# Optimization experiments

Hardware: AMD Instinct MI355X
Metric: run time of the kernel (lower is better)

The kernel has to match this reference:

```python
import jax, jax.numpy as jnp
import numpy as np

E = 1024
H = 16
D = E // H  # head_dim = 64
FF = 4 * E
EPS = 1e-5


def layernorm(x, g, b):
    mu = jnp.mean(x, axis=-1, keepdims=True)
    var = jnp.var(x, axis=-1, keepdims=True)
    return (x - mu) * jax.lax.rsqrt(var + EPS) * g + b


def setup_inputs() -> dict:
    key = jax.random.key(0)
    ks = jax.random.split(key, 12)
    s = 1.0 / np.sqrt(E)
    sf = 1.0 / np.sqrt(FF)
    return {
        "x": jax.random.normal(ks[0], (2, 2048, E), dtype=jnp.float32),
        "wq": jax.random.uniform(ks[1], (E, E), jnp.float32, -s, s),
        "wk": jax.random.uniform(ks[2], (E, E), jnp.float32, -s, s),
        "wv": jax.random.uniform(ks[3], (E, E), jnp.float32, -s, s),
        "wo": jax.random.uniform(ks[4], (E, E), jnp.float32, -s, s),
        "bo": jax.random.uniform(ks[5], (E,), jnp.float32, -s, s),
        "g1": jnp.ones((E,), jnp.float32),
        "b1": jnp.zeros((E,), jnp.float32),
        "w1": jax.random.uniform(ks[6], (FF, E), jnp.float32, -s, s),
        "bf1": jax.random.uniform(ks[7], (FF,), jnp.float32, -s, s),
        "w2": jax.random.uniform(ks[8], (E, FF), jnp.float32, -sf, sf),
        "bf2": jax.random.uniform(ks[9], (E,), jnp.float32, -sf, sf),
        "g2": jnp.ones((E,), jnp.float32),
        "b2": jnp.zeros((E,), jnp.float32),
    }


def reference(x, wq, wk, wv, wo, bo, g1, b1, w1, bf1, w2, bf2, g2, b2):
    B, L, _ = x.shape
    # projections (torch Linear: x @ W.T)
    q = (x @ wq.T).reshape(B, L, H, D).transpose(0, 2, 1, 3)  # (B,H,L,D)
    k = (x @ wk.T).reshape(B, L, H, D).transpose(0, 2, 1, 3)
    v = (x @ wv.T).reshape(B, L, H, D).transpose(0, 2, 1, 3)
    scores = jnp.einsum('bhqd,bhkd->bhqk', q, k) / np.sqrt(D)
    attn = jax.nn.softmax(scores, axis=-1)
    ctx = jnp.einsum('bhqk,bhkd->bhqd', attn, v)
    ctx = ctx.transpose(0, 2, 1, 3).reshape(B, L, E)
    attn_out = ctx @ wo.T + bo
    h = layernorm(x + attn_out, g1, b1)
    ff = jax.nn.gelu(h @ w1.T + bf1, approximate=False) @ w2.T + bf2
    return layernorm(h + ff, g2, b2)
```

## Files before the change

### kernel.cpp

```cpp
#include <hip/hip_runtime.h>
#include <hip/hip_bf16.h>
#include <stdint.h>

typedef __bf16 bf16x8 __attribute__((ext_vector_type(8)));
typedef float  f32x4  __attribute__((ext_vector_type(4)));
typedef unsigned short u16;
typedef u16 u16x8 __attribute__((ext_vector_type(8)));

__device__ __forceinline__ u16 f2b(float f) {
  uint32_t u = __builtin_bit_cast(uint32_t, f);
  u += 0x7fffu + ((u >> 16) & 1u);
  return (u16)(u >> 16);
}

__device__ __forceinline__ f32x4 mfma16(bf16x8 a, bf16x8 b, f32x4 c) {
  return __builtin_amdgcn_mfma_f32_16x16x32_bf16(a, b, c, 0, 0, 0);
}

__device__ __forceinline__ void gload_lds16(const void* g, void* l) {
  __builtin_amdgcn_global_load_lds(
      (const __attribute__((address_space(1))) void*)g,
      (__attribute__((address_space(3))) void*)l, 16, 0, 0);
}

__global__ void f2b_all(const float* __restrict__ x,  const float* __restrict__ wq,
                        const float* __restrict__ wk, const float* __restrict__ wv,
                        const float* __restrict__ wo, const float* __restrict__ w1,
                        const float* __restrict__ w2,
                        u16* __restrict__ xb, u16* __restrict__ wqkvb,
                        u16* __restrict__ wob, u16* __restrict__ w1b,
                        u16* __restrict__ w2b) {
  const int i = blockIdx.x * blockDim.x + threadIdx.x;
  const float* src; u16* dst; int off;
  if (i < 524288)        { src = x;  dst = xb;              off = i; }
  else if (i < 655360)   { src = wq; dst = wqkvb;           off = i - 524288; }
  else if (i < 786432)   { src = wk; dst = wqkvb + 1048576; off = i - 655360; }
  else if (i < 917504)   { src = wv; dst = wqkvb + 2097152; off = i - 786432; }
  else if (i < 1048576)  { src = wo; dst = wob;             off = i - 917504; }
  else if (i < 1572864)  { src = w1; dst = w1b;             off = i - 1048576; }
  else                   { src = w2; dst = w2b;             off = i - 1572864; }
  const float4* p = (const float4*)src + (size_t)off * 2;
  float4 a = p[0], b = p[1];
  u16x8 r;
  r[0] = f2b(a.x); r[1] = f2b(a.y); r[2] = f2b(a.z); r[3] = f2b(a.w);
  r[4] = f2b(b.x); r[5] = f2b(b.y); r[6] = f2b(b.z); r[7] = f2b(b.w);
  *((u16x8*)dst + off) = r;
}

template<int MODE>
__global__ __launch_bounds__(256, 3) void gemm_bt(
    const u16* __restrict__ A, const u16* __restrict__ W,
    const float* __restrict__ bias,
    void* __restrict__ o0, void* __restrict__ o1, void* __restrict__ o2,
    int Nsz, int Kstride, int Klen, int ntiles)
{
  __shared__ u16 As[2][128 * 32];
  __shared__ u16 Bs[2][128 * 32];
  const int nbn = Nsz >> 7;
  int bid = blockIdx.x;
  bid = (bid & 7) * ((int)gridDim.x >> 3) + (bid >> 3);
  const int tile = (MODE == 1) ? (bid % ntiles) : bid;
  const int sid  = (MODE == 1) ? (bid / ntiles) : 0;
  const int koff = sid * Klen;
  const int bm = tile / nbn;
  const int bn = tile % nbn;
  const int tid = threadIdx.x;
  const int w = tid >> 6, l = tid & 63;
  const int lh = l >> 4, ll = l & 15;
  const int wr = w >> 1, wc = w & 1;

  f32x4 acc[4][4] = {};

  const u16* Ag = A + (size_t)(bm * 128) * Kstride + koff;
  const u16* Wg = W + (size_t)(bn * 128) * Kstride + koff;

  const int flat0 = (w * 2) * 64 + l;
  const int flat1 = (w * 2 + 1) * 64 + l;

  {
    gload_lds16(Ag + (size_t)(flat0 >> 2) * Kstride + (flat0 & 3) * 8, As[0] + flat0 * 8);
    gload_lds16(Wg + (size_t)(flat0 >> 2) * Kstride + (flat0 & 3) * 8, Bs[0] + flat0 * 8);
    gload_lds16(Ag + (size_t)(flat1 >> 2) * Kstride + (flat1 & 3) * 8, As[0] + flat1 * 8);
    gload_lds16(Wg + (size_t)(flat1 >> 2) * Kstride + (flat1 & 3) * 8, Bs[0] + flat1 * 8);
  }
  __syncthreads();

  const int NS = Klen >> 5;
  int buf = 0;
  for (int s = 0; s < NS; ++s) {
    if (s + 1 < NS) {
      const int k0 = (s + 1) * 32;
      gload_lds16(Ag + (size_t)(flat0 >> 2) * Kstride + k0 + (flat0 & 3) * 8, As[buf ^ 1] + flat0 * 8);
      gload_lds16(Wg + (size_t)(flat0 >> 2) * Kstride + k0 + (flat0 & 3) * 8, Bs[buf ^ 1] + flat0 * 8);
      gload_lds16(Ag + (size_t)(flat1 >> 2) * Kstride + k0 + (flat1 & 3) * 8, As[buf ^ 1] + flat1 * 8);
      gload_lds16(Wg + (size_t)(flat1 >> 2) * Kstride + k0 + (flat1 & 3) * 8, Bs[buf ^ 1] + flat1 * 8);
    }
    bf16x8 af[4], bfr[4];
#pragma unroll
    for (int mi = 0; mi < 4; ++mi)
      af[mi] = *(const bf16x8*)(As[buf] + (wr * 64 + mi * 16 + ll) * 32 + lh * 8);
#pragma unroll
    for (int ni = 0; ni < 4; ++ni)
      bfr[ni] = *(const bf16x8*)(Bs[buf] + (wc * 64 + ni * 16 + ll) * 32 + lh * 8);
    __builtin_amdgcn_s_setprio(1);
#pragma unroll
    for (int mi = 0; mi < 4; ++mi)
#pragma unroll
      for (int ni = 0; ni < 4; ++ni)
        acc[mi][ni] = mfma16(af[mi], bfr[ni], acc[mi][ni]);
    __builtin_amdgcn_s_setprio(0);
    __syncthreads();
    buf ^= 1;
  }

#pragma unroll
  for (int mi = 0; mi < 4; ++mi) {
#pragma unroll
    for (int ni = 0; ni < 4; ++ni) {
      const int col = bn * 128 + wc * 64 + ni * 16 + ll;
#pragma unroll
      for (int i = 0; i < 4; ++i) {
        const int row = bm * 128 + wr * 64 + mi * 16 + lh * 4 + i;
        float v = acc[mi][ni][i];
        if (MODE == 1) {
          float* dst = sid ? (float*)o1 : (float*)o0;
          dst[(size_t)row * Nsz + col] = v;
        } else if (MODE == 2) {
          float xx = v + bias[col];
          float u = xx * (0.7978845608f + 0.0356774081f * xx * xx);
          float t = __builtin_amdgcn_exp2f(u * 2.8853900818f);
          float r = __builtin_amdgcn_rcpf(1.0f + t);
          ((u16*)o0)[(size_t)row * Nsz + col] = f2b(xx * t * r);
        } else {
          const int which = col >> 10;
          const int e = col & 1023;
          const int hh = e >> 6, dd = e & 63;
          const int bb = row >> 11, nl = row & 2047;
          if (which == 0) {
            ((u16*)o0)[((size_t)(bb * 16 + hh) * 2048 + nl) * 64 + dd] = f2b(v * 0.18033688f);
          } else if (which == 1) {
            ((u16*)o1)[((size_t)(bb * 16 + hh) * 2048 + nl) * 64 + dd] = f2b(v);
          } else {
            ((u16*)o2)[((size_t)(bb * 16 + hh) * 64 + dd) * 2048 + nl] = f2b(v);
          }
        }
      }
    }
  }
}

__global__ __launch_bounds__(256, 3) void attn_fwd(
    const u16* __restrict__ Q, const u16* __restrict__ K,
    const u16* __restrict__ Vt, u16* __restrict__ ctx)
{
  __shared__ u16 Ks[2][64 * 64];
  __shared__ u16 Vs[2][64 * 64];
  __shared__ u16 Ps[4][32 * 64];

  const int bh = blockIdx.x & 31;
  const int qt = blockIdx.x >> 5;
  const int tid = threadIdx.x;
  const int w = tid >> 6, l = tid & 63;
  const int lh = l >> 4, ll = l & 15;
  const int q0 = qt * 128 + w * 32;

  bf16x8 qf[2][2];
#pragma unroll
  for (int qh = 0; qh < 2; ++qh) {
    const u16* Qg = Q + ((size_t)bh * 2048 + q0 + qh * 16 + ll) * 64;
#pragma unroll
    for (int kk = 0; kk < 2; ++kk)
      qf[qh][kk] = *(const bf16x8*)(Qg + kk * 32 + lh * 8);
  }

  bf16x8 ones;
  {
    const u16 o = 0x3F80;
#pragma unroll
    for (int i = 0; i < 8; ++i) ones[i] = __builtin_bit_cast(__bf16, o);
  }

  f32x4 cacc[2][4] = {};
  f32x4 lacc[2] = {};
  float m_l[2] = {-1e30f, -1e30f};
  u16* ps = Ps[w];

  const int f0 = tid, f1 = 256 + tid;
  const int r0 = f0 >> 3, s0 = f0 & 7, g0 = (s0 ^ (r0 & 7)) * 8;
  const int r1 = f1 >> 3, s1 = f1 & 7, g1 = (s1 ^ (r1 & 7)) * 8;

  {
    gload_lds16(K + ((size_t)bh * 2048 + r0) * 64 + g0, Ks[0] + f0 * 8);
    gload_lds16(Vt + ((size_t)bh * 64 + r0) * 2048 + g0, Vs[0] + f0 * 8);
    gload_lds16(K + ((size_t)bh * 2048 + r1) * 64 + g1, Ks[0] + f1 * 8);
    gload_lds16(Vt + ((size_t)bh * 64 + r1) * 2048 + g1, Vs[0] + f1 * 8);
  }
  __syncthreads();

  for (int kt = 0; kt < 32; ++kt) {
    const int b = kt & 1;
    if (kt < 31) {
      const int kn = (kt + 1) * 64;
      gload_lds16(K + ((size_t)bh * 2048 + kn + r0) * 64 + g0, Ks[b ^ 1] + f0 * 8);
      gload_lds16(Vt + ((size_t)bh * 64 + r0) * 2048 + kn + g0, Vs[b ^ 1] + f0 * 8);
      gload_lds16(K + ((size_t)bh * 2048 + kn + r1) * 64 + g1, Ks[b ^ 1] + f1 * 8);
      gload_lds16(Vt + ((size_t)bh * 64 + r1) * 2048 + kn + g1, Vs[b ^ 1] + f1 * 8);
    }

    f32x4 st[2][4];
    __builtin_amdgcn_s_setprio(1);
#pragma unroll
    for (int jb = 0; jb < 4; ++jb) {
      f32x4 a0 = {}, a1 = {};
#pragma unroll
      for (int kk = 0; kk < 2; ++kk) {
        const int r = jb * 16 + ll;
        bf16x8 kf = *(const bf16x8*)(Ks[b] + r * 64 + (((kk * 4 + lh) ^ (r & 7)) * 8));
        a0 = mfma16(kf, qf[0][kk], a0);
        a1 = mfma16(kf, qf[1][kk], a1);
      }
      st[0][jb] = a0; st[1][jb] = a1;
    }
    __builtin_amdgcn_s_setprio(0);

    float mx[2];
#pragma unroll
    for (int qh = 0; qh < 2; ++qh) {
      float m = fmaxf(fmaxf(fmaxf(st[qh][0][0], st[qh][0][1]), fmaxf(st[qh][0][2], st[qh][0][3])),
                      fmaxf(fmaxf(st[qh][1][0], st[qh][1][1]), fmaxf(st[qh][1][2], st[qh][1][3])));
      m = fmaxf(m, fmaxf(fmaxf(fmaxf(st[qh][2][0], st[qh][2][1]), fmaxf(st[qh][2][2], st[qh][2][3])),
                         fmaxf(fmaxf(st[qh][3][0], st[qh][3][1]), fmaxf(st[qh][3][2], st[qh][3][3]))));
      m = fmaxf(m, __shfl_xor(m, 16));
      m = fmaxf(m, __shfl_xor(m, 32));
      mx[qh] = m;
    }

    if (!__all(mx[0] - m_l[0] <= 8.0f && mx[1] - m_l[1] <= 8.0f)) {
#pragma unroll
      for (int qh = 0; qh < 2; ++qh) {
        const float mn = fmaxf(m_l[qh], mx[qh]);
        const float al = __builtin_amdgcn_exp2f(m_l[qh] - mn);
        m_l[qh] = mn;
        float alq[4];
#pragma unroll
        for (int i = 0; i < 4; ++i) alq[i] = __shfl(al, lh * 4 + i);
#pragma unroll
        for (int db = 0; db < 4; ++db)
#pragma unroll
          for (int i = 0; i < 4; ++i) cacc[qh][db][i] *= alq[i];
#pragma unroll
        for (int i = 0; i < 4; ++i) lacc[qh][i] *= alq[i];
      }
    }

#pragma unroll
    for (int qh = 0; qh < 2; ++qh)
#pragma unroll
      for (int jb = 0; jb < 4; ++jb) {
        const float p0 = __builtin_amdgcn_exp2f(st[qh][jb][0] - m_l[qh]);
        const float p1 = __builtin_amdgcn_exp2f(st[qh][jb][1] - m_l[qh]);
        const float p2 = __builtin_amdgcn_exp2f(st[qh][jb][2] - m_l[qh]);
        const float p3 = __builtin_amdgcn_exp2f(st[qh][jb][3] - m_l[qh]);
        uint2 pk;
        asm("v_cvt_pk_bf16_f32 %0, %1, %2" : "=v"(pk.x) : "v"(p0), "v"(p1));
        asm("v_cvt_pk_bf16_f32 %0, %1, %2" : "=v"(pk.y) : "v"(p2), "v"(p3));
        *(uint2*)(ps + (qh * 16 + ll) * 64 +
                  (((jb * 2 + (lh >> 1)) ^ (ll & 7)) * 8) + (lh & 1) * 4) = pk;
      }

    asm volatile("s_waitcnt lgkmcnt(0)" ::: "memory");
    __builtin_amdgcn_sched_barrier(0);

    __builtin_amdgcn_s_setprio(1);
#pragma unroll
    for (int kk = 0; kk < 2; ++kk) {
      bf16x8 pf0 = *(const bf16x8*)(ps + ll * 64 + (((kk * 4 + lh) ^ (ll & 7)) * 8));
      bf16x8 pf1 = *(const bf16x8*)(ps + (16 + ll) * 64 + (((kk * 4 + lh) ^ (ll & 7)) * 8));
      lacc[0] = mfma16(pf0, ones, lacc[0]);
      lacc[1] = mfma16(pf1, ones, lacc[1]);
#pragma unroll
      for (int db = 0; db < 4; ++db) {
        const int vr = db * 16 + ll;
        bf16x8 vf = *(const bf16x8*)(Vs[b] + vr * 64 + (((kk * 4 + lh) ^ (vr & 7)) * 8));
        cacc[0][db] = mfma16(pf0, vf, cacc[0][db]);
        cacc[1][db] = mfma16(pf1, vf, cacc[1][db]);
      }
    }
    __builtin_amdgcn_s_setprio(0);
    __syncthreads();
  }

  const int bb = bh >> 4, hh = bh & 15;
#pragma unroll
  for (int qh = 0; qh < 2; ++qh)
#pragma unroll
    for (int db = 0; db < 4; ++db)
#pragma unroll
      for (int i = 0; i < 4; ++i) {
        const float v = cacc[qh][db][i] / lacc[qh][i];
        const size_t orow = (size_t)bb * 2048 + q0 + qh * 16 + lh * 4 + i;
        const size_t ocol = (size_t)hh * 64 + db * 16 + ll;
        ctx[orow * 1024 + ocol] = f2b(v);
      }
}

__global__ __launch_bounds__(256) void ln_fused(
    const float* __restrict__ a,  const float* __restrict__ b0,
    const float* __restrict__ b1, const float* __restrict__ b2,
    const float* __restrict__ b3, const float* __restrict__ bias,
    const float* __restrict__ g,  const float* __restrict__ be,
    float* __restrict__ ho, u16* __restrict__ hb)
{
  const int row = blockIdx.x;
  const int t = threadIdx.x;
  const size_t base = (size_t)row * 1024 + t * 4;
  float4 xa = *(const float4*)(a + base);
  float4 xb = *(const float4*)(b0 + base);
  float v0 = xa.x + xb.x, v1 = xa.y + xb.y, v2 = xa.z + xb.z, v3 = xa.w + xb.w;
  if (b1) {
    float4 xc = *(const float4*)(b1 + base);
    v0 += xc.x; v1 += xc.y; v2 += xc.z; v3 += xc.w;
  }
  if (b2) {
    float4 xc = *(const float4*)(b2 + base);
    v0 += xc.x; v1 += xc.y; v2 += xc.z; v3 += xc.w;
  }
  if (b3) {
    float4 xc = *(const float4*)(b3 + base);
    v0 += xc.x; v1 += xc.y; v2 += xc.z; v3 += xc.w;
  }
  if (bias) {
    float4 xd = *(const float4*)(bias + t * 4);
    v0 += xd.x; v1 += xd.y; v2 += xd.z; v3 += xd.w;
  }
  float s = v0 + v1 + v2 + v3;
  float ss = v0 * v0 + v1 * v1 + v2 * v2 + v3 * v3;
#pragma unroll
  for (int d = 1; d < 64; d <<= 1) {
    s += __shfl_xor(s, d);
    ss += __shfl_xor(ss, d);
  }
  __shared__ float red[8];
  const int w = t >> 6, lid = t & 63;
  if (lid == 0) { red[w] = s; red[4 + w] = ss; }
  __syncthreads();
  s = red[0] + red[1] + red[2] + red[3];
  ss = red[4] + red[5] + red[6] + red[7];
  const float mean = s * (1.0f / 1024.0f);
  const float var = ss * (1.0f / 1024.0f) - mean * mean;
  const float rstd = rsqrtf(var + 1e-5f);
  const float vv[4] = {v0, v1, v2, v3};
#pragma unroll
  for (int i = 0; i < 4; ++i) {
    const int col = t * 4 + i;
    const float hv = (vv[i] - mean) * rstd * g[col] + be[col];
    if (ho) ho[base + i] = hv;
    if (hb) hb[base + i] = f2b(hv);
  }
}

extern "C" void kernel_launch(void* const* d_in, const int* in_sizes, int n_in,
                              void* d_out, int out_size, void* d_ws, size_t ws_size,
                              hipStream_t stream) {
  const float* x   = (const float*)d_in[0];
  const float* wq  = (const float*)d_in[1];
  const float* wk  = (const float*)d_in[2];
  const float* wv  = (const float*)d_in[3];
  const float* wo  = (const float*)d_in[4];
  const float* bo  = (const float*)d_in[5];
  const float* g1  = (const float*)d_in[6];
  const float* b1  = (const float*)d_in[7];
  const float* w1  = (const float*)d_in[8];
  const float* bf1 = (const float*)d_in[9];
  const float* w2  = (const float*)d_in[10];
  const float* bf2 = (const float*)d_in[11];
  const float* g2  = (const float*)d_in[12];
  const float* b2  = (const float*)d_in[13];

  char* ws = (char*)d_ws;
  const size_t MB = 1u << 20;
  u16* xb    = (u16*)(ws + 0);
  u16* wqkv  = (u16*)(ws + 8 * MB);
  u16* wob   = (u16*)(ws + 14 * MB);
  u16* w1b   = (u16*)(ws + 16 * MB);
  u16* w2b   = (u16*)(ws + 24 * MB);
  u16* qb    = (u16*)(ws + 32 * MB);
  u16* kb    = (u16*)(ws + 40 * MB);
  u16* vtb   = (u16*)(ws + 48 * MB);
  u16* ctxb  = (u16*)(ws + 56 * MB);
  float* pA   = (float*)(ws + 64 * MB);
  float* hbuf = (float*)(ws + 80 * MB);
  u16* hbb   = (u16*)(ws + 96 * MB);
  float* wo_p1 = (float*)(ws + 32 * MB);
  u16* ff1   = (u16*)(ws + 32 * MB);
  float* f2_p1 = (float*)(ws + 0);

  f2b_all<<<8192, 256, 0, stream>>>(x, wq, wk, wv, wo, w1, w2, xb, wqkv, wob, w1b, w2b);

  gemm_bt<0><<<768, 256, 0, stream>>>(xb, wqkv, nullptr, qb, kb, vtb, 3072, 1024, 1024, 768);
  attn_fwd<<<512, 256, 0, stream>>>(qb, kb, vtb, ctxb);
  gemm_bt<1><<<512, 256, 0, stream>>>(ctxb, wob, nullptr, pA, wo_p1, nullptr, 1024, 1024, 512, 256);
  ln_fused<<<4096, 256, 0, stream>>>(x, pA, wo_p1, nullptr, nullptr, bo, g1, b1, hbuf, hbb);
  gemm_bt<2><<<1024, 256, 0, stream>>>(hbb, w1b, bf1, ff1, nullptr, nullptr, 4096, 1024, 1024, 1024);
  gemm_bt<1><<<512, 256, 0, stream>>>(ff1, w2b, nullptr, pA, f2_p1, nullptr, 1024, 4096, 2048, 256);
  ln_fused<<<4096, 256, 0, stream>>>(hbuf, pA, f2_p1, nullptr, nullptr, bf2, g2, b2,
                                     (float*)d_out, nullptr);
}
```

Baseline: 255.7 us.

## Split attention over two key halves and merge partial softmax results

```diff
diff --git a/kernel.cpp b/kernel.cpp
--- a/kernel.cpp
+++ b/kernel.cpp
@@ -151,18 +151,22 @@
 
 __global__ __launch_bounds__(256, 3) void attn_fwd(
     const u16* __restrict__ Q, const u16* __restrict__ K,
-    const u16* __restrict__ Vt, u16* __restrict__ ctx)
+    const u16* __restrict__ Vt, float* __restrict__ Opart,
+    float* __restrict__ ml)
 {
   __shared__ u16 Ks[2][64 * 64];
   __shared__ u16 Vs[2][64 * 64];
   __shared__ u16 Ps[4][32 * 64];
 
-  const int bh = blockIdx.x & 31;
-  const int qt = blockIdx.x >> 5;
+  const int bq = blockIdx.x & 511;
+  const int ks = blockIdx.x >> 9;
+  const int bh = bq & 31;
+  const int qt = bq >> 5;
   const int tid = threadIdx.x;
   const int w = tid >> 6, l = tid & 63;
   const int lh = l >> 4, ll = l & 15;
   const int q0 = qt * 128 + w * 32;
+  const int kbase = ks * 16;
 
   bf16x8 qf[2][2];
 #pragma unroll
@@ -190,17 +194,18 @@
   const int r1 = f1 >> 3, s1 = f1 & 7, g1 = (s1 ^ (r1 & 7)) * 8;
 
   {
-    gload_lds16(K + ((size_t)bh * 2048 + r0) * 64 + g0, Ks[0] + f0 * 8);
-    gload_lds16(Vt + ((size_t)bh * 64 + r0) * 2048 + g0, Vs[0] + f0 * 8);
-    gload_lds16(K + ((size_t)bh * 2048 + r1) * 64 + g1, Ks[0] + f1 * 8);
-    gload_lds16(Vt + ((size_t)bh * 64 + r1) * 2048 + g1, Vs[0] + f1 * 8);
+    const int kn = kbase * 64;
+    gload_lds16(K + ((size_t)bh * 2048 + kn + r0) * 64 + g0, Ks[0] + f0 * 8);
+    gload_lds16(Vt + ((size_t)bh * 64 + r0) * 2048 + kn + g0, Vs[0] + f0 * 8);
+    gload_lds16(K + ((size_t)bh * 2048 + kn + r1) * 64 + g1, Ks[0] + f1 * 8);
+    gload_lds16(Vt + ((size_t)bh * 64 + r1) * 2048 + kn + g1, Vs[0] + f1 * 8);
   }
   __syncthreads();
 
-  for (int kt = 0; kt < 32; ++kt) {
+  for (int kt = 0; kt < 16; ++kt) {
     const int b = kt & 1;
-    if (kt < 31) {
-      const int kn = (kt + 1) * 64;
+    if (kt < 15) {
+      const int kn = (kbase + kt + 1) * 64;
       gload_lds16(K + ((size_t)bh * 2048 + kn + r0) * 64 + g0, Ks[b ^ 1] + f0 * 8);
       gload_lds16(Vt + ((size_t)bh * 64 + r0) * 2048 + kn + g0, Vs[b ^ 1] + f0 * 8);
       gload_lds16(K + ((size_t)bh * 2048 + kn + r1) * 64 + g1, Ks[b ^ 1] + f1 * 8);
@@ -290,18 +295,53 @@
     __syncthreads();
   }
 
-  const int bb = bh >> 4, hh = bh & 15;
-#pragma unroll
-  for (int qh = 0; qh < 2; ++qh)
+  const size_t obase = (size_t)(ks * 32 + bh) * 2048;
+#pragma unroll
+  for (int qh = 0; qh < 2; ++qh) {
+    float mq[4];
+#pragma unroll
+    for (int i = 0; i < 4; ++i) mq[i] = __shfl(m_l[qh], lh * 4 + i);
+    if (ll == 0) {
+#pragma unroll
+      for (int i = 0; i < 4; ++i) {
+        const int q = q0 + qh * 16 + lh * 4 + i;
+        ((float2*)ml)[obase + q] = make_float2(mq[i], lacc[qh][i]);
+      }
+    }
 #pragma unroll
     for (int db = 0; db < 4; ++db)
 #pragma unroll
       for (int i = 0; i < 4; ++i) {
-        const float v = cacc[qh][db][i] / lacc[qh][i];
-        const size_t orow = (size_t)bb * 2048 + q0 + qh * 16 + lh * 4 + i;
-        const size_t ocol = (size_t)hh * 64 + db * 16 + ll;
-        ctx[orow * 1024 + ocol] = f2b(v);
-      }
+        const int q = q0 + qh * 16 + lh * 4 + i;
+        Opart[(obase + q) * 64 + db * 16 + ll] = cacc[qh][db][i];
+      }
+  }
+}
+
+__global__ __launch_bounds__(256) void attn_merge(
+    const float* __restrict__ Opart, const float* __restrict__ ml,
+    u16* __restrict__ ctx)
+{
+  const int r = blockIdx.x * 16 + (threadIdx.x >> 4);
+  const int d0 = (threadIdx.x & 15) * 4;
+  const float2 a = ((const float2*)ml)[r];
+  const float2 bm = ((const float2*)ml)[65536 + r];
+  const float M = fmaxf(a.x, bm.x);
+  const float w0 = __builtin_amdgcn_exp2f(a.x - M);
+  const float w1 = __builtin_amdgcn_exp2f(bm.x - M);
+  const float dn = 1.0f / (a.y * w0 + bm.y * w1);
+  const float4 o0 = *(const float4*)(Opart + (size_t)r * 64 + d0);
+  const float4 o1 = *(const float4*)(Opart + ((size_t)65536 + r) * 64 + d0);
+  const float v0 = (o0.x * w0 + o1.x * w1) * dn;
+  const float v1 = (o0.y * w0 + o1.y * w1) * dn;
+  const float v2 = (o0.z * w0 + o1.z * w1) * dn;
+  const float v3 = (o0.w * w0 + o1.w * w1) * dn;
+  const int bh = r >> 11, q = r & 2047;
+  u16* dst = ctx + ((size_t)(bh >> 4) * 2048 + q) * 1024 + (bh & 15) * 64 + d0;
+  uint2 pk;
+  pk.x = (uint32_t)f2b(v0) | ((uint32_t)f2b(v1) << 16);
+  pk.y = (uint32_t)f2b(v2) | ((uint32_t)f2b(v3) << 16);
+  *(uint2*)dst = pk;
 }
 
 __global__ __launch_bounds__(256) void ln_fused(
@@ -388,6 +428,8 @@
   u16* kb    = (u16*)(ws + 40 * MB);
   u16* vtb   = (u16*)(ws + 48 * MB);
   u16* ctxb  = (u16*)(ws + 56 * MB);
+  float* Opart = (float*)(ws + 64 * MB);
+  float* mlb   = (float*)(ws + 96 * MB);
   float* pA   = (float*)(ws + 64 * MB);
   float* hbuf = (float*)(ws + 80 * MB);
   u16* hbb   = (u16*)(ws + 96 * MB);
@@ -398,7 +440,8 @@
   f2b_all<<<8192, 256, 0, stream>>>(x, wq, wk, wv, wo, w1, w2, xb, wqkv, wob, w1b, w2b);
 
   gemm_bt<0><<<768, 256, 0, stream>>>(xb, wqkv, nullptr, qb, kb, vtb, 3072, 1024, 1024, 768);
-  attn_fwd<<<512, 256, 0, stream>>>(qb, kb, vtb, ctxb);
+  attn_fwd<<<1024, 256, 0, stream>>>(qb, kb, vtb, Opart, mlb);
+  attn_merge<<<4096, 256, 0, stream>>>(Opart, mlb, ctxb);
   gemm_bt<1><<<512, 256, 0, stream>>>(ctxb, wob, nullptr, pA, wo_p1, nullptr, 1024, 1024, 512, 256);
   ln_fused<<<4096, 256, 0, stream>>>(x, pA, wo_p1, nullptr, nullptr, bo, g1, b1, hbuf, hbb);
   gemm_bt<2><<<1024, 256, 0, stream>>>(hbb, w1b, bf1, ff1, nullptr, nullptr, 4096, 1024, 1024, 1024);
```

Result: slower. 266.8 us (+4.4%).
